# Kernel tuning notes

Hardware: AMD Instinct MI355X
Metric: run time of the kernel (lower is better)

Reference implementation:

```python
import jax, jax.numpy as jnp
import numpy as np
import math

HIDDEN = 2048
N_HEADS = 32
N_KV_HEADS = 8
HEAD_DIM = HIDDEN // N_HEADS  # 64
N_REP = N_HEADS // N_KV_HEADS  # 4
ROPE_THETA = 10000.0
BSZ, SEQ = 2, 2048


def setup_inputs() -> dict:
    key = jax.random.key(0)
    ks = jax.random.split(key, 6)
    hidden_states = jax.random.normal(ks[0], (BSZ, SEQ, HIDDEN), dtype=jnp.float32)
    wq = jax.random.normal(ks[1], (HIDDEN, N_HEADS * HEAD_DIM), dtype=jnp.float32) * (HIDDEN ** -0.5)
    wk = jax.random.normal(ks[2], (HIDDEN, N_KV_HEADS * HEAD_DIM), dtype=jnp.float32) * (HIDDEN ** -0.5)
    wv = jax.random.normal(ks[3], (HIDDEN, N_KV_HEADS * HEAD_DIM), dtype=jnp.float32) * (HIDDEN ** -0.5)
    wo = jax.random.normal(ks[4], (N_HEADS * HEAD_DIM, HIDDEN), dtype=jnp.float32) * (HIDDEN ** -0.5)
    # additive causal mask [b, 1, q, kv]
    neg = jnp.finfo(jnp.float32).min
    causal = jnp.where(jnp.tril(jnp.ones((SEQ, SEQ), dtype=bool)), 0.0, neg)
    attention_mask = jnp.broadcast_to(causal[None, None], (BSZ, 1, SEQ, SEQ)).astype(jnp.float32)
    position_ids = jnp.broadcast_to(jnp.arange(SEQ, dtype=jnp.int32)[None], (BSZ, SEQ))
    return {
        "hidden_states": hidden_states,
        "wq": wq, "wk": wk, "wv": wv, "wo": wo,
        "attention_mask": attention_mask,
        "position_ids": position_ids,
    }


def _rope_cache(seq_len, dtype):
    inv_freq = 1.0 / (ROPE_THETA ** (jnp.arange(0, HEAD_DIM, 2, dtype=jnp.float32) / HEAD_DIM))
    t = jnp.arange(seq_len, dtype=jnp.float32)
    freqs = jnp.outer(t, inv_freq)              # [S, head_dim/2]
    emb = jnp.concatenate([freqs, freqs], -1)   # [S, head_dim]
    return jnp.cos(emb).astype(dtype), jnp.sin(emb).astype(dtype)


def _rotate_half(x):
    x1, x2 = jnp.split(x, 2, axis=-1)
    return jnp.concatenate([-x2, x1], axis=-1)


def reference(hidden_states, wq, wk, wv, wo, attention_mask, position_ids):
    b, s, _ = hidden_states.shape
    q = (hidden_states @ wq).reshape(b, s, N_HEADS, HEAD_DIM).transpose(0, 2, 1, 3)
    k = (hidden_states @ wk).reshape(b, s, N_KV_HEADS, HEAD_DIM).transpose(0, 2, 1, 3)
    v = (hidden_states @ wv).reshape(b, s, N_KV_HEADS, HEAD_DIM).transpose(0, 2, 1, 3)

    cos_c, sin_c = _rope_cache(s, hidden_states.dtype)
    cos = cos_c[position_ids][:, None]  # [b,1,s,head_dim]
    sin = sin_c[position_ids][:, None]
    q = q * cos + _rotate_half(q) * sin
    k = k * cos + _rotate_half(k) * sin

    # repeat_kv: [b, kvh, s, d] -> [b, kvh*n_rep, s, d]
    k = jnp.broadcast_to(k[:, :, None], (b, N_KV_HEADS, N_REP, s, HEAD_DIM)).reshape(b, N_HEADS, s, HEAD_DIM)
    v = jnp.broadcast_to(v[:, :, None], (b, N_KV_HEADS, N_REP, s, HEAD_DIM)).reshape(b, N_HEADS, s, HEAD_DIM)

    scores = jnp.einsum('bhqd,bhkd->bhqk', q, k) / math.sqrt(HEAD_DIM)
    scores = scores + attention_mask
    probs = jax.nn.softmax(scores.astype(jnp.float32), axis=-1).astype(q.dtype)
    attn = jnp.einsum('bhqk,bhkd->bhqd', probs, v)  # [b,h,s,d]
    attn = attn.transpose(0, 2, 1, 3).reshape(b, s, N_HEADS * HEAD_DIM)
    return attn @ wo
```

## Files before the change

### kernel.cpp

```cpp
#include <hip/hip_runtime.h>
#include <math.h>


typedef float f32x4 __attribute__((ext_vector_type(4)));
typedef short s16x8 __attribute__((ext_vector_type(8)));
typedef unsigned short u16x4 __attribute__((ext_vector_type(4)));

__device__ __forceinline__ unsigned short f2bf(float x) {
    union { float f; unsigned int u; } v; v.f = x;
    unsigned int r = v.u + 0x7FFF + ((v.u >> 16) & 1);
    return (unsigned short)(r >> 16);
}

__global__ __launch_bounds__(256) void prep(
    const float* __restrict__ X, const float* __restrict__ Wq,
    const float* __restrict__ Wk, const float* __restrict__ Wv,
    const float* __restrict__ Wo,
    unsigned short* __restrict__ Xb, unsigned short* __restrict__ Wqkvt,
    unsigned short* __restrict__ Wot) {
    const int bid = blockIdx.x;
    if (bid < 8192) {
        size_t i = (size_t)bid * 256 + threadIdx.x;
        f32x4 v = *(const f32x4*)&X[i * 4];
        u16x4 r;
        r[0] = f2bf(v[0]); r[1] = f2bf(v[1]); r[2] = f2bf(v[2]); r[3] = f2bf(v[3]);
        *(u16x4*)&Xb[i * 4] = r;
        return;
    }
    __shared__ float t[32][33];
    const int tb = bid - 8192;
    const int kbi = tb / 160, bx = tb - kbi * 160;
    const float* W; unsigned short* Out; int N, n0, nb;
    if (bx < 64)      { W = Wq; Out = Wqkvt; N = 2048; n0 = 0;    nb = bx; }
    else if (bx < 80) { W = Wk; Out = Wqkvt; N = 512;  n0 = 2048; nb = bx - 64; }
    else if (bx < 96) { W = Wv; Out = Wqkvt; N = 512;  n0 = 2560; nb = bx - 80; }
    else              { W = Wo; Out = Wot;   N = 2048; n0 = 0;    nb = bx - 96; }
    int kb = kbi * 32; nb *= 32;
    int tx = threadIdx.x & 31, ty = threadIdx.x >> 5;
#pragma unroll
    for (int i = 0; i < 4; ++i)
        t[ty + i * 8][tx] = W[(size_t)(kb + ty + i * 8) * N + nb + tx];
    __syncthreads();
#pragma unroll
    for (int i = 0; i < 4; ++i)
        Out[(size_t)(n0 + nb + ty + i * 8) * 2048 + kb + tx] = f2bf(t[tx][ty + i * 8]);
}

__global__ __launch_bounds__(256) void gemm_qkv_rope(
    const unsigned short* __restrict__ A, const unsigned short* __restrict__ Bt,
    const int* __restrict__ pos,
    unsigned short* __restrict__ Qb, unsigned short* __restrict__ Kb,
    unsigned short* __restrict__ Vb) {
    const int K = 2048;
    __shared__ unsigned short As[128 * 64];
    __shared__ unsigned short Bs[128 * 64];
    const int tid = threadIdx.x;
    const int wave = tid >> 6, lane = tid & 63;
    const int col = lane & 15, quad = lane >> 4;
    const int m0 = blockIdx.y * 128, n0 = blockIdx.x * 128;
    const int wm = (wave >> 1) * 64, wn = (wave & 1) * 64;

    const int lrow = lane >> 3;
    const int gch = (lane & 7) ^ lrow;
    const unsigned short* Ag = A + (size_t)(m0 + wave * 32 + lrow) * K + gch * 8;
    const unsigned short* Bg = Bt + (size_t)(n0 + wave * 32 + lrow) * K + gch * 8;
    unsigned short* AsW = As + wave * 2048;
    unsigned short* BsW = Bs + wave * 2048;

    f32x4 acc[4][4] = {};

    for (int k0 = 0; k0 < K; k0 += 64) {
#pragma unroll
        for (int i = 0; i < 4; ++i) {
            __builtin_amdgcn_global_load_lds(
                (const __attribute__((address_space(1))) void*)(Ag + (size_t)i * 8 * K + k0),
                (__attribute__((address_space(3))) void*)(AsW + i * 512), 16, 0, 0);
            __builtin_amdgcn_global_load_lds(
                (const __attribute__((address_space(1))) void*)(Bg + (size_t)i * 8 * K + k0),
                (__attribute__((address_space(3))) void*)(BsW + i * 512), 16, 0, 0);
        }
        __syncthreads();
#pragma unroll
        for (int ks = 0; ks < 2; ++ks) {
            const int slot = ((ks << 2) + quad) ^ (col & 7);
            s16x8 af[4], bf[4];
#pragma unroll
            for (int mi = 0; mi < 4; ++mi)
                af[mi] = *(const s16x8*)&As[(wm + mi * 16 + col) * 64 + slot * 8];
#pragma unroll
            for (int ni = 0; ni < 4; ++ni)
                bf[ni] = *(const s16x8*)&Bs[(wn + ni * 16 + col) * 64 + slot * 8];
#pragma unroll
            for (int mi = 0; mi < 4; ++mi)
#pragma unroll
                for (int ni = 0; ni < 4; ++ni)
                    acc[mi][ni] = __builtin_amdgcn_mfma_f32_16x16x32_bf16(
                        af[mi], bf[ni], acc[mi][ni], 0, 0, 0);
        }
        __syncthreads();
    }

    const int cb = n0 + wn;
    if (cb >= 2560) {
        const int hd = (cb - 2560) >> 6;
#pragma unroll
        for (int mi = 0; mi < 4; ++mi)
#pragma unroll
            for (int r = 0; r < 4; ++r) {
                int m = m0 + wm + mi * 16 + quad * 4 + r;
                int b = m >> 11, s = m & 2047;
                size_t rb = ((size_t)(b * 8 + hd) * 2048 + s) * 64;
#pragma unroll
                for (int ni = 0; ni < 4; ++ni)
                    Vb[rb + ni * 16 + col] = f2bf(acc[mi][ni][r]);
            }
    } else {
        const int isQ = (cb < 2048);
        const int hd = isQ ? (cb >> 6) : ((cb - 2048) >> 6);
        const int nh = isQ ? 32 : 8;
        const float scale = isQ ? 0.125f : 1.0f;
        unsigned short* Out = isQ ? Qb : Kb;
        const float NEG_LN_TH_32 = -0.28782313662425575f;
        const float inv0 = __expf((float)col * NEG_LN_TH_32);
        const float inv1 = __expf((float)(col + 16) * NEG_LN_TH_32);
#pragma unroll
        for (int mi = 0; mi < 4; ++mi)
#pragma unroll
            for (int r = 0; r < 4; ++r) {
                int m = m0 + wm + mi * 16 + quad * 4 + r;
                int b = m >> 11, s = m & 2047;
                float p = (float)pos[m];
                float sn0, cs0, sn1, cs1;
                __sincosf(p * inv0, &sn0, &cs0);
                __sincosf(p * inv1, &sn1, &cs1);
                float a0 = acc[mi][0][r], a1 = acc[mi][1][r];
                float b0 = acc[mi][2][r], b1 = acc[mi][3][r];
                size_t rb = ((size_t)(b * nh + hd) * 2048 + s) * 64;
                Out[rb + col]      = f2bf((a0 * cs0 - b0 * sn0) * scale);
                Out[rb + col + 16] = f2bf((a1 * cs1 - b1 * sn1) * scale);
                Out[rb + col + 32] = f2bf((b0 * cs0 + a0 * sn0) * scale);
                Out[rb + col + 48] = f2bf((b1 * cs1 + a1 * sn1) * scale);
            }
    }
}

__global__ __launch_bounds__(256) void gemm_bf16_nt(
    const unsigned short* __restrict__ A, const unsigned short* __restrict__ Bt,
    float* __restrict__ C, int K, int ldc) {
    __shared__ unsigned short As[128 * 64];
    __shared__ unsigned short Bs[128 * 64];
    const int tid = threadIdx.x;
    const int wave = tid >> 6, lane = tid & 63;
    const int col = lane & 15, quad = lane >> 4;
    const int m0 = blockIdx.y * 128, n0 = blockIdx.x * 128;
    const int wm = (wave >> 1) * 64, wn = (wave & 1) * 64;

    const int lrow = lane >> 3;
    const int gch = (lane & 7) ^ lrow;
    const unsigned short* Ag = A + (size_t)(m0 + wave * 32 + lrow) * K + gch * 8;
    const unsigned short* Bg = Bt + (size_t)(n0 + wave * 32 + lrow) * K + gch * 8;
    unsigned short* AsW = As + wave * 2048;
    unsigned short* BsW = Bs + wave * 2048;

    f32x4 acc[4][4] = {};

    for (int k0 = 0; k0 < K; k0 += 64) {
#pragma unroll
        for (int i = 0; i < 4; ++i) {
            __builtin_amdgcn_global_load_lds(
                (const __attribute__((address_space(1))) void*)(Ag + (size_t)i * 8 * K + k0),
                (__attribute__((address_space(3))) void*)(AsW + i * 512), 16, 0, 0);
            __builtin_amdgcn_global_load_lds(
                (const __attribute__((address_space(1))) void*)(Bg + (size_t)i * 8 * K + k0),
                (__attribute__((address_space(3))) void*)(BsW + i * 512), 16, 0, 0);
        }
        __syncthreads();
#pragma unroll
        for (int ks = 0; ks < 2; ++ks) {
            const int slot = ((ks << 2) + quad) ^ (col & 7);
            s16x8 af[4], bf[4];
#pragma unroll
            for (int mi = 0; mi < 4; ++mi)
                af[mi] = *(const s16x8*)&As[(wm + mi * 16 + col) * 64 + slot * 8];
#pragma unroll
            for (int ni = 0; ni < 4; ++ni)
                bf[ni] = *(const s16x8*)&Bs[(wn + ni * 16 + col) * 64 + slot * 8];
#pragma unroll
            for (int mi = 0; mi < 4; ++mi)
#pragma unroll
                for (int ni = 0; ni < 4; ++ni)
                    acc[mi][ni] = __builtin_amdgcn_mfma_f32_16x16x32_bf16(
                        af[mi], bf[ni], acc[mi][ni], 0, 0, 0);
        }
        __syncthreads();
    }
#pragma unroll
    for (int mi = 0; mi < 4; ++mi)
#pragma unroll
        for (int ni = 0; ni < 4; ++ni)
#pragma unroll
            for (int r = 0; r < 4; ++r) {
                int m = m0 + wm + mi * 16 + quad * 4 + r;
                int n = n0 + wn + ni * 16 + col;
                C[(size_t)m * ldc + n] = acc[mi][ni][r];
            }
}

__global__ __launch_bounds__(256) void transpose_v(
    const unsigned short* __restrict__ Vb, unsigned short* __restrict__ Vt) {
    __shared__ unsigned short t[64 * 66];
    const int bh = blockIdx.x >> 5, st = blockIdx.x & 31;
    const unsigned short* src = Vb + ((size_t)bh * 2048 + st * 64) * 64;
    unsigned short* dst = Vt + (size_t)bh * 64 * 2048 + st * 64;
    const int r = threadIdx.x >> 2, c = (threadIdx.x & 3) * 16;
    s16x8 v0 = *(const s16x8*)&src[r * 64 + c];
    s16x8 v1 = *(const s16x8*)&src[r * 64 + c + 8];
    unsigned* tw = (unsigned*)&t[r * 66 + c];
#pragma unroll
    for (int q2 = 0; q2 < 4; ++q2) tw[q2] = ((unsigned*)&v0)[q2];
#pragma unroll
    for (int q2 = 0; q2 < 4; ++q2) tw[4 + q2] = ((unsigned*)&v1)[q2];
    __syncthreads();
    const int d = threadIdx.x >> 2, sc2 = (threadIdx.x & 3) * 16;
    unsigned short outv[16];
#pragma unroll
    for (int jj = 0; jj < 16; ++jj) outv[jj] = t[(sc2 + jj) * 66 + d];
    *(s16x8*)&dst[(size_t)d * 2048 + sc2] = *(s16x8*)&outv[0];
    *(s16x8*)&dst[(size_t)d * 2048 + sc2 + 8] = *(s16x8*)&outv[8];
}

__global__ __launch_bounds__(128, 2) void flash_attn(
    const unsigned short* __restrict__ Qb, const unsigned short* __restrict__ Kb,
    const unsigned short* __restrict__ Vt, unsigned short* __restrict__ Ob) {
    __shared__ unsigned short Ks[64 * 64];
    __shared__ unsigned short Vs[64 * 64];
    __shared__ unsigned short PsA[2][32 * 64];
    __shared__ unsigned short PsB[2][32 * 64];

    const int tid = threadIdx.x;
    const int wave = tid >> 6, lane = tid & 63;
    const int col = lane & 15, quad = lane >> 4;

    const int id = blockIdx.x;
    const int j = ((id & 15) + ((id >> 8) << 2)) & 15;
    const int bh = id >> 4;
    const int b = bh >> 5, h = bh & 31, kvh = h >> 2;
    const int qA0 = (31 - j) * 64, qB0 = j * 64;
    const int qwA = qA0 + wave * 32, qwB = qB0 + wave * 32;

    const unsigned short* Qg  = Qb + ((size_t)(b * 32 + h) * 2048) * 64;
    const unsigned short* Kgb = Kb + ((size_t)(b * 8 + kvh) * 2048) * 64;
    const unsigned short* Vgb = Vt + ((size_t)(b * 8 + kvh) * 64) * 2048;

    const int r8 = lane >> 3, g = (lane & 7) ^ r8;
    const unsigned short* KgL = Kgb + (size_t)(wave * 32 + r8) * 64 + g * 8;
    const unsigned short* VgL = Vgb + (size_t)(wave * 32 + r8) * 2048 + g * 8;
    unsigned short* KsW = Ks + wave * 32 * 64;
    unsigned short* VsW = Vs + wave * 32 * 64;

    const s16x8 onesf = {16256, 16256, 16256, 16256, 16256, 16256, 16256, 16256};

    s16x8 qfA[2][2], qfB[2][2];
#pragma unroll
    for (int qc = 0; qc < 2; ++qc)
#pragma unroll
        for (int ks = 0; ks < 2; ++ks) {
            qfA[qc][ks] = *(const s16x8*)&Qg[(size_t)(qwA + qc * 16 + col) * 64 + ks * 32 + quad * 8];
            qfB[qc][ks] = *(const s16x8*)&Qg[(size_t)(qwB + qc * 16 + col) * 64 + ks * 32 + quad * 8];
        }

    f32x4 aoA[2][4] = {}, aoB[2][4] = {};
    f32x4 alA[2] = {}, alB[2] = {};

    for (int kv0 = 0; kv0 <= qA0; kv0 += 64) {
#pragma unroll
        for (int i = 0; i < 4; ++i) {
            __builtin_amdgcn_global_load_lds(
                (const __attribute__((address_space(1))) void*)(KgL + (size_t)(kv0 + i * 8) * 64),
                (__attribute__((address_space(3))) void*)(KsW + i * 512), 16, 0, 0);
            __builtin_amdgcn_global_load_lds(
                (const __attribute__((address_space(1))) void*)(VgL + kv0 + (size_t)i * 8 * 2048),
                (__attribute__((address_space(3))) void*)(VsW + i * 512), 16, 0, 0);
        }
        __syncthreads();
        const bool doB = (kv0 <= qB0);
#pragma unroll
        for (int mi = 0; mi < 4; ++mi) {
            const int s0 = quad ^ (col & 7);
            const int s1 = (4 + quad) ^ (col & 7);
            s16x8 kf0 = *(const s16x8*)&Ks[(mi * 16 + col) * 64 + s0 * 8];
            s16x8 kf1 = *(const s16x8*)&Ks[(mi * 16 + col) * 64 + s1 * 8];
            const int chl = (mi * 2 + (quad >> 1)) ^ (col & 7);
#pragma unroll
            for (int qc = 0; qc < 2; ++qc) {
                f32x4 sc = {};
                sc = __builtin_amdgcn_mfma_f32_16x16x32_bf16(kf0, qfA[qc][0], sc, 0, 0, 0);
                sc = __builtin_amdgcn_mfma_f32_16x16x32_bf16(kf1, qfA[qc][1], sc, 0, 0, 0);
                if (kv0 == qA0) {
                    int kvb = kv0 + mi * 16 + quad * 4, q = qwA + qc * 16 + col;
#pragma unroll
                    for (int r = 0; r < 4; ++r)
                        if (kvb + r > q) sc[r] = -1e30f;
                }
                unsigned eb[4];
#pragma unroll
                for (int r = 0; r < 4; ++r) eb[r] = __float_as_uint(__expf(sc[r]));
                uint2 pk;
                pk.x = __builtin_amdgcn_perm(eb[1], eb[0], 0x07060302u);
                pk.y = __builtin_amdgcn_perm(eb[3], eb[2], 0x07060302u);
                *(uint2*)&PsA[wave][(qc * 16 + col) * 64 + chl * 8 + (quad & 1) * 4] = pk;
            }
            if (doB) {
#pragma unroll
                for (int qc = 0; qc < 2; ++qc) {
                    f32x4 sc = {};
                    sc = __builtin_amdgcn_mfma_f32_16x16x32_bf16(kf0, qfB[qc][0], sc, 0, 0, 0);
                    sc = __builtin_amdgcn_mfma_f32_16x16x32_bf16(kf1, qfB[qc][1], sc, 0, 0, 0);
                    if (kv0 == qB0) {
                        int kvb = kv0 + mi * 16 + quad * 4, q = qwB + qc * 16 + col;
#pragma unroll
                        for (int r = 0; r < 4; ++r)
                            if (kvb + r > q) sc[r] = -1e30f;
                    }
                    unsigned eb[4];
#pragma unroll
                    for (int r = 0; r < 4; ++r) eb[r] = __float_as_uint(__expf(sc[r]));
                    uint2 pk;
                    pk.x = __builtin_amdgcn_perm(eb[1], eb[0], 0x07060302u);
                    pk.y = __builtin_amdgcn_perm(eb[3], eb[2], 0x07060302u);
                    *(uint2*)&PsB[wave][(qc * 16 + col) * 64 + chl * 8 + (quad & 1) * 4] = pk;
                }
            }
        }
        asm volatile("s_waitcnt lgkmcnt(0)" ::: "memory");
#pragma unroll
        for (int ks = 0; ks < 2; ++ks) {
            const int slot = ((ks << 2) + quad) ^ (col & 7);
            s16x8 vf[4];
#pragma unroll
            for (int di = 0; di < 4; ++di)
                vf[di] = *(const s16x8*)&Vs[(di * 16 + col) * 64 + slot * 8];
#pragma unroll
            for (int qc = 0; qc < 2; ++qc) {
                s16x8 pfA = *(const s16x8*)&PsA[wave][(qc * 16 + col) * 64 + slot * 8];
                alA[qc] = __builtin_amdgcn_mfma_f32_16x16x32_bf16(pfA, onesf, alA[qc], 0, 0, 0);
#pragma unroll
                for (int di = 0; di < 4; ++di)
                    aoA[qc][di] = __builtin_amdgcn_mfma_f32_16x16x32_bf16(pfA, vf[di], aoA[qc][di], 0, 0, 0);
            }
            if (doB) {
#pragma unroll
                for (int qc = 0; qc < 2; ++qc) {
                    s16x8 pfB = *(const s16x8*)&PsB[wave][(qc * 16 + col) * 64 + slot * 8];
                    alB[qc] = __builtin_amdgcn_mfma_f32_16x16x32_bf16(pfB, onesf, alB[qc], 0, 0, 0);
#pragma unroll
                    for (int di = 0; di < 4; ++di)
                        aoB[qc][di] = __builtin_amdgcn_mfma_f32_16x16x32_bf16(pfB, vf[di], aoB[qc][di], 0, 0, 0);
                }
            }
        }
        __syncthreads();
    }

#pragma unroll
    for (int qc = 0; qc < 2; ++qc)
#pragma unroll
        for (int r = 0; r < 4; ++r) {
            {
                int qg = qwA + qc * 16 + quad * 4 + r;
                float inv = 1.f / alA[qc][r];
                size_t base = ((size_t)b * 2048 + qg) * 2048 + h * 64;
#pragma unroll
                for (int di = 0; di < 4; ++di)
                    Ob[base + di * 16 + col] = f2bf(aoA[qc][di][r] * inv);
            }
            {
                int qg = qwB + qc * 16 + quad * 4 + r;
                float inv = 1.f / alB[qc][r];
                size_t base = ((size_t)b * 2048 + qg) * 2048 + h * 64;
#pragma unroll
                for (int di = 0; di < 4; ++di)
                    Ob[base + di * 16 + col] = f2bf(aoB[qc][di][r] * inv);
            }
        }
}

extern "C" void kernel_launch(void* const* d_in, const int* in_sizes, int n_in,
                              void* d_out, int out_size, void* d_ws, size_t ws_size,
                              hipStream_t stream) {
    const float* X  = (const float*)d_in[0];
    const float* Wq = (const float*)d_in[1];
    const float* Wk = (const float*)d_in[2];
    const float* Wv = (const float*)d_in[3];
    const float* Wo = (const float*)d_in[4];
    const int* pos  = (const int*)d_in[6];
    float* out = (float*)d_out;

    char* ws = (char*)d_ws;
    unsigned short* Xb    = (unsigned short*)(ws + 0);
    unsigned short* Wqkvt = (unsigned short*)(ws + 16777216);
    unsigned short* Wot   = (unsigned short*)(ws + 29360128);
    unsigned short* Qb    = (unsigned short*)(ws + 37748736);
    unsigned short* Kb    = (unsigned short*)(ws + 54525952);
    unsigned short* Vb    = (unsigned short*)(ws + 58720256);
    unsigned short* Vt    = (unsigned short*)(ws + 62914560);
    unsigned short* Attn  = Xb;

    prep<<<18432, 256, 0, stream>>>(X, Wq, Wk, Wv, Wo, Xb, Wqkvt, Wot);
    gemm_qkv_rope<<<dim3(24, 32), 256, 0, stream>>>(Xb, Wqkvt, pos, Qb, Kb, Vb);
    transpose_v<<<512, 256, 0, stream>>>(Vb, Vt);
    flash_attn<<<1024, 128, 0, stream>>>(Qb, Kb, Vt, Attn);
    gemm_bf16_nt<<<dim3(16, 32), 256, 0, stream>>>(Attn, Wot, out, 2048, 2048);
}
```

Before: 315.9 us.

## Fuse V transpose into QKV GEMM epilogue and shrink output GEMM tile

The QKV GEMM epilogue now stages V tiles through swizzled shared memory and writes V directly in transposed layout. This removes the separate transpose kernel and its extra global read and write of V. The output projection GEMM switches to a 128x64 tile with launch bounds of 4 waves, doubling the grid from 512 to 1024 blocks for better CU fill. In exchange each A tile is reloaded for twice as many column blocks. The epilogue relies on each wave only touching its own LDS region, with an lgkmcnt wait instead of a barrier.

```diff
diff --git a/kernel.cpp b/kernel.cpp
--- a/kernel.cpp
+++ b/kernel.cpp
@@ -50,7 +50,7 @@
     const unsigned short* __restrict__ A, const unsigned short* __restrict__ Bt,
     const int* __restrict__ pos,
     unsigned short* __restrict__ Qb, unsigned short* __restrict__ Kb,
-    unsigned short* __restrict__ Vb) {
+    unsigned short* __restrict__ Vt) {
     const int K = 2048;
     __shared__ unsigned short As[128 * 64];
     __shared__ unsigned short Bs[128 * 64];
@@ -103,17 +103,30 @@
     const int cb = n0 + wn;
     if (cb >= 2560) {
         const int hd = (cb - 2560) >> 6;
+        unsigned short* t = (wave < 2) ? (As + wave * 4096) : (Bs + (wave - 2) * 4096);
 #pragma unroll
         for (int mi = 0; mi < 4; ++mi)
 #pragma unroll
-            for (int r = 0; r < 4; ++r) {
-                int m = m0 + wm + mi * 16 + quad * 4 + r;
-                int b = m >> 11, s = m & 2047;
-                size_t rb = ((size_t)(b * 8 + hd) * 2048 + s) * 64;
-#pragma unroll
-                for (int ni = 0; ni < 4; ++ni)
-                    Vb[rb + ni * 16 + col] = f2bf(acc[mi][ni][r]);
-            }
+            for (int ni = 0; ni < 4; ++ni)
+#pragma unroll
+                for (int r = 0; r < 4; ++r) {
+                    int sl = mi * 16 + quad * 4 + r;
+                    int d  = ni * 16 + col;
+                    int ch = (sl >> 3) ^ (d & 7);
+                    t[d * 64 + ch * 8 + (sl & 7)] = f2bf(acc[mi][ni][r]);
+                }
+        asm volatile("s_waitcnt lgkmcnt(0)" ::: "memory");
+        const int b = m0 >> 11;
+        const int s0 = (m0 & 2047) + wm;
+        unsigned short* dst = Vt + ((size_t)(b * 8 + hd) * 64) * 2048 + s0;
+        const int c = lane & 7;
+#pragma unroll
+        for (int it = 0; it < 8; ++it) {
+            int d = it * 8 + (lane >> 3);
+            int ch = c ^ (d & 7);
+            s16x8 v = *(const s16x8*)&t[d * 64 + ch * 8];
+            *(s16x8*)&dst[(size_t)d * 2048 + c * 8] = v;
+        }
     } else {
         const int isQ = (cb < 2048);
         const int hd = isQ ? (cb >> 6) : ((cb - 2048) >> 6);
@@ -144,51 +157,53 @@
     }
 }
 
-__global__ __launch_bounds__(256) void gemm_bf16_nt(
+__global__ __launch_bounds__(256, 4) void gemm2_nt(
     const unsigned short* __restrict__ A, const unsigned short* __restrict__ Bt,
-    float* __restrict__ C, int K, int ldc) {
+    float* __restrict__ C) {
+    const int K = 2048, ldc = 2048;
     __shared__ unsigned short As[128 * 64];
-    __shared__ unsigned short Bs[128 * 64];
+    __shared__ unsigned short Bs[64 * 64];
     const int tid = threadIdx.x;
     const int wave = tid >> 6, lane = tid & 63;
     const int col = lane & 15, quad = lane >> 4;
-    const int m0 = blockIdx.y * 128, n0 = blockIdx.x * 128;
-    const int wm = (wave >> 1) * 64, wn = (wave & 1) * 64;
+    const int m0 = blockIdx.y * 128, n0 = blockIdx.x * 64;
+    const int wm = (wave >> 1) * 64, wn = (wave & 1) * 32;
 
     const int lrow = lane >> 3;
     const int gch = (lane & 7) ^ lrow;
     const unsigned short* Ag = A + (size_t)(m0 + wave * 32 + lrow) * K + gch * 8;
-    const unsigned short* Bg = Bt + (size_t)(n0 + wave * 32 + lrow) * K + gch * 8;
+    const unsigned short* Bg = Bt + (size_t)(n0 + wave * 16 + lrow) * K + gch * 8;
     unsigned short* AsW = As + wave * 2048;
-    unsigned short* BsW = Bs + wave * 2048;
-
-    f32x4 acc[4][4] = {};
+    unsigned short* BsW = Bs + wave * 1024;
+
+    f32x4 acc[4][2] = {};
 
     for (int k0 = 0; k0 < K; k0 += 64) {
 #pragma unroll
-        for (int i = 0; i < 4; ++i) {
+        for (int i = 0; i < 4; ++i)
             __builtin_amdgcn_global_load_lds(
                 (const __attribute__((address_space(1))) void*)(Ag + (size_t)i * 8 * K + k0),
                 (__attribute__((address_space(3))) void*)(AsW + i * 512), 16, 0, 0);
+#pragma unroll
+        for (int i = 0; i < 2; ++i)
             __builtin_amdgcn_global_load_lds(
                 (const __attribute__((address_space(1))) void*)(Bg + (size_t)i * 8 * K + k0),
                 (__attribute__((address_space(3))) void*)(BsW + i * 512), 16, 0, 0);
-        }
         __syncthreads();
 #pragma unroll
         for (int ks = 0; ks < 2; ++ks) {
             const int slot = ((ks << 2) + quad) ^ (col & 7);
-            s16x8 af[4], bf[4];
+            s16x8 af[4], bf[2];
 #pragma unroll
             for (int mi = 0; mi < 4; ++mi)
                 af[mi] = *(const s16x8*)&As[(wm + mi * 16 + col) * 64 + slot * 8];
 #pragma unroll
-            for (int ni = 0; ni < 4; ++ni)
+            for (int ni = 0; ni < 2; ++ni)
                 bf[ni] = *(const s16x8*)&Bs[(wn + ni * 16 + col) * 64 + slot * 8];
 #pragma unroll
             for (int mi = 0; mi < 4; ++mi)
 #pragma unroll
-                for (int ni = 0; ni < 4; ++ni)
+                for (int ni = 0; ni < 2; ++ni)
                     acc[mi][ni] = __builtin_amdgcn_mfma_f32_16x16x32_bf16(
                         af[mi], bf[ni], acc[mi][ni], 0, 0, 0);
         }
@@ -197,36 +212,13 @@
 #pragma unroll
     for (int mi = 0; mi < 4; ++mi)
 #pragma unroll
-        for (int ni = 0; ni < 4; ++ni)
+        for (int ni = 0; ni < 2; ++ni)
 #pragma unroll
             for (int r = 0; r < 4; ++r) {
                 int m = m0 + wm + mi * 16 + quad * 4 + r;
                 int n = n0 + wn + ni * 16 + col;
                 C[(size_t)m * ldc + n] = acc[mi][ni][r];
             }
-}
-
-__global__ __launch_bounds__(256) void transpose_v(
-    const unsigned short* __restrict__ Vb, unsigned short* __restrict__ Vt) {
-    __shared__ unsigned short t[64 * 66];
-    const int bh = blockIdx.x >> 5, st = blockIdx.x & 31;
-    const unsigned short* src = Vb + ((size_t)bh * 2048 + st * 64) * 64;
-    unsigned short* dst = Vt + (size_t)bh * 64 * 2048 + st * 64;
-    const int r = threadIdx.x >> 2, c = (threadIdx.x & 3) * 16;
-    s16x8 v0 = *(const s16x8*)&src[r * 64 + c];
-    s16x8 v1 = *(const s16x8*)&src[r * 64 + c + 8];
-    unsigned* tw = (unsigned*)&t[r * 66 + c];
-#pragma unroll
-    for (int q2 = 0; q2 < 4; ++q2) tw[q2] = ((unsigned*)&v0)[q2];
-#pragma unroll
-    for (int q2 = 0; q2 < 4; ++q2) tw[4 + q2] = ((unsigned*)&v1)[q2];
-    __syncthreads();
-    const int d = threadIdx.x >> 2, sc2 = (threadIdx.x & 3) * 16;
-    unsigned short outv[16];
-#pragma unroll
-    for (int jj = 0; jj < 16; ++jj) outv[jj] = t[(sc2 + jj) * 66 + d];
-    *(s16x8*)&dst[(size_t)d * 2048 + sc2] = *(s16x8*)&outv[0];
-    *(s16x8*)&dst[(size_t)d * 2048 + sc2 + 8] = *(s16x8*)&outv[8];
 }
 
 __global__ __launch_bounds__(128, 2) void flash_attn(
@@ -402,13 +394,11 @@
     unsigned short* Wot   = (unsigned short*)(ws + 29360128);
     unsigned short* Qb    = (unsigned short*)(ws + 37748736);
     unsigned short* Kb    = (unsigned short*)(ws + 54525952);
-    unsigned short* Vb    = (unsigned short*)(ws + 58720256);
-    unsigned short* Vt    = (unsigned short*)(ws + 62914560);
+    unsigned short* Vt    = (unsigned short*)(ws + 58720256);
     unsigned short* Attn  = Xb;
 
     prep<<<18432, 256, 0, stream>>>(X, Wq, Wk, Wv, Wo, Xb, Wqkvt, Wot);
-    gemm_qkv_rope<<<dim3(24, 32), 256, 0, stream>>>(Xb, Wqkvt, pos, Qb, Kb, Vb);
-    transpose_v<<<512, 256, 0, stream>>>(Vb, Vt);
+    gemm_qkv_rope<<<dim3(24, 32), 256, 0, stream>>>(Xb, Wqkvt, pos, Qb, Kb, Vt);
     flash_attn<<<1024, 128, 0, stream>>>(Qb, Kb, Vt, Attn);
-    gemm_bf16_nt<<<dim3(16, 32), 256, 0, stream>>>(Attn, Wot, out, 2048, 2048);
-}
+    gemm2_nt<<<dim3(32, 32), 256, 0, stream>>>(Attn, Wot, out);
+}
```

After: 320.8 us. No clear change (+1.6%).
